# Performance work log

Measured on AMD Instinct MI355X. Metric: run time of the kernel, lower is better.

## Reference

```python
import jax, jax.numpy as jnp
import numpy as np

REF_POSE = np.array([[213.33335876464844, 124.50563049316406], [190.504638671875, 115.11840057373047], [169.9791717529297, 101.77180480957031], [146.72341918945312, 96.25749206542969], [128.86770629882812, 87.2344970703125], [150.34292602539062, 101.61070251464844], [119.29926300048828, 98.73982238769531], [100.03463745117188, 99.74459838867188], [82.62400817871094, 101.2509536743164], [148.91049194335938, 112.71517181396484], [114.37303161621094, 113.20121002197266], [91.90096282958984, 116.49812316894531], [74.75020599365234, 119.37875366210938], [149.59658813476562, 124.09295654296875], [119.72419738769531, 126.36898040771484], [99.59107208251953, 129.40196228027344], [82.82524108886719, 131.584228515625], [154.55911254882812, 135.07681274414062], [133.8833770751953, 140.85983276367188], [120.45906066894531, 145.40306091308594], [106.21541595458984, 150.072265625]], dtype=np.float32)

SCALES = (0.25, 0.5, 1.0)
ORIENTATIONS = (0, 90, 180, 270)
INPUT_SIZE = (256, 256)          # (H, W)
ANCHOR_STRIDE = (1, 1)           # (y_stride, x_stride)
POS_TH = 0.5
KPT_SIGMA = 0.05                 # per-keypoint OKS falloff


def _generate_anchor_poses():
    # scale + rotate ref pose about its centroid -> [A, 21, 2]
    c = REF_POSE.mean(axis=0, keepdims=True)
    out = []
    for s in SCALES:
        for o in ORIENTATIONS:
            th = np.deg2rad(o)
            R = np.array([[np.cos(th), -np.sin(th)], [np.sin(th), np.cos(th)]], dtype=np.float32)
            out.append(c + s * (REF_POSE - c) @ R.T)
    return np.stack(out).astype(np.float32)


def _all_anchors(feat_h, feat_w):
    base = _generate_anchor_poses()                      # [A,21,2]
    w_ratio = INPUT_SIZE[1] / feat_w
    h_ratio = INPUT_SIZE[0] / feat_h
    sx = np.arange(0, feat_w, ANCHOR_STRIDE[1]) * w_ratio
    sy = np.arange(0, feat_h, ANCHOR_STRIDE[0]) * h_ratio
    gx, gy = np.meshgrid(sx, sy)
    shifts = np.stack([gx.ravel(), gy.ravel()], axis=1).astype(np.float32)  # [K,2]
    all_a = base[None, :, :, :] + shifts[:, None, None, :]                  # [K,A,21,2]
    return jnp.asarray(all_a.reshape(-1, 21, 2))                            # [K*A,21,2]


def _pose_oks(anchors, gt):
    # anchors [N,21,2], gt [B,2,21,3] -> OKS sim [B,N,2]
    d2 = jnp.sum((anchors[None, :, None, :, :] - gt[:, None, :, :, :2]) ** 2, axis=-1)  # [B,N,2,21]
    vis = (gt[..., 2] > 0).astype(anchors.dtype)[:, None, :, :]                          # [B,1,2,21]
    xy = gt[..., :2]
    area = jnp.prod(xy.max(axis=2) - xy.min(axis=2), axis=-1)                            # [B,2]
    s2 = jnp.maximum(area, 1.0)[:, None, :, None]                                        # [B,1,2,1]
    k2 = (2.0 * KPT_SIGMA) ** 2
    oks = jnp.exp(-d2 / (2.0 * s2 * k2))
    return jnp.sum(oks * vis, axis=-1) / jnp.maximum(jnp.sum(vis, axis=-1), 1.0)          # [B,N,2]


def setup_inputs() -> dict:
    key = jax.random.key(0)
    k1, k2 = jax.random.split(key)
    B = 16
    xy = jax.random.uniform(k1, (B, 42, 2), dtype=jnp.float32) * 216.0 + 20.0
    vis = jnp.ones((B, 42, 1), dtype=jnp.float32)
    pose_gt = jnp.concatenate([xy, vis], axis=-1)          # [B,42,3]
    hand_type = jnp.ones((B, 2), dtype=jnp.int32)          # both hands present
    return {"pose_gt": pose_gt, "hand_type": hand_type, "feat_h": 64, "feat_w": 64}


def reference(pose_gt, hand_type, feat_h, feat_w):
    all_anchors = _all_anchors(feat_h, feat_w)             # [N,21,2], N=K*A
    inside = jnp.sum((all_anchors[..., 0] >= 0) & (all_anchors[..., 1] >= 0)
                     & (all_anchors[..., 0] < INPUT_SIZE[0])
                     & (all_anchors[..., 1] < INPUT_SIZE[1]), axis=1) == 21  # [N]

    B = pose_gt.shape[0]
    gt = pose_gt.reshape(B, 2, 21, 3)                      # hand 0 = right, hand 1 = left
    sim = _pose_oks(all_anchors, gt)                       # [B,N,2]
    am = jnp.argmax(sim, axis=-1)                          # [B,N]
    mx = jnp.max(sim, axis=-1)                             # [B,N]

    right = (am == 0) & (mx > POS_TH) & (hand_type[:, 0:1] == 1) & inside[None, :]
    left = (am == 1) & (mx > POS_TH) & (hand_type[:, 1:2] == 1) & inside[None, :]
    neg = (~right) & (~left) & inside[None, :]

    # labels channel layout matches source: [:,:,0]=left, [:,:,1]=negative, [:,:,2]=right
    labels = jnp.stack([left, neg, right], axis=-1).astype(pose_gt.dtype)   # [B,N,3]
    labels = jnp.where(inside[None, :, None], labels, jnp.asarray(-1.0, pose_gt.dtype))

    pose_targets = (jnp.where(right[..., None, None], gt[:, 0][:, None], 0.0)
                    + jnp.where(left[..., None, None], gt[:, 1][:, None], 0.0))  # [B,N,21,3]

    offsets = pose_targets[..., :2] - all_anchors[None, :, :, :]             # [B,N,21,2]
    offsets = jnp.where(inside[None, :, None, None], offsets, 0.0)
    return all_anchors, inside, labels, offsets
```

## Files before the change

kernel.cpp:

```cpp
#include <hip/hip_runtime.h>
#include <math.h>

#define NA 49152
#define NB 16
#define ABLOCKS 192
#define EPS 1e-3f
#define OF4B 516096
#define OF4  8257536
#define AF4  516096
#define IF4  12288

__device__ __forceinline__ void st4(float* p, float a, float b, float c, float d) {
  *reinterpret_cast<float4*>(p) = make_float4(a, b, c, d);
}

__constant__ float RP[21][2] = {
  {213.33335876464844f, 124.50563049316406f},
  {190.504638671875f,   115.11840057373047f},
  {169.9791717529297f,  101.77180480957031f},
  {146.72341918945312f, 96.25749206542969f},
  {128.86770629882812f, 87.2344970703125f},
  {150.34292602539062f, 101.61070251464844f},
  {119.29926300048828f, 98.73982238769531f},
  {100.03463745117188f, 99.74459838867188f},
  {82.62400817871094f,  101.2509536743164f},
  {148.91049194335938f, 112.71517181396484f},
  {114.37303161621094f, 113.20121002197266f},
  {91.90096282958984f,  116.49812316894531f},
  {74.75020599365234f,  119.37875366210938f},
  {149.59658813476562f, 124.09295654296875f},
  {119.72419738769531f, 126.36898040771484f},
  {99.59107208251953f,  129.40196228027344f},
  {82.82524108886719f,  131.584228515625f},
  {154.55911254882812f, 135.07681274414062f},
  {133.8833770751953f,  140.85983276367188f},
  {120.45906066894531f, 145.40306091308594f},
  {106.21541595458984f, 150.072265625f}
};

__device__ __forceinline__ void ref_center(float& cx, float& cy) {
  #pragma clang fp contract(off)
  float rx[8], ry[8];
  #pragma unroll
  for (int j = 0; j < 8; ++j) {
    rx[j] = RP[j][0] + RP[j + 8][0];
    ry[j] = RP[j][1] + RP[j + 8][1];
  }
  float sx = ((rx[0] + rx[1]) + (rx[2] + rx[3])) + ((rx[4] + rx[5]) + (rx[6] + rx[7]));
  float sy = ((ry[0] + ry[1]) + (ry[2] + ry[3])) + ((ry[4] + ry[5]) + (ry[6] + ry[7]));
  #pragma unroll
  for (int j = 16; j < 21; ++j) { sx += RP[j][0]; sy += RP[j][1]; }
  cx = sx / 21.0f;
  cy = sy / 21.0f;
}

__device__ __forceinline__ float2 base_pt(int p, int j, float cx, float cy) {
  #pragma clang fp contract(off)
  const int si = p >> 2, oi = p & 3;
  const float s = (si == 0) ? 0.25f : (si == 1 ? 0.5f : 1.0f);
  const float dx = s * (RP[j][0] - cx);
  const float dy = s * (RP[j][1] - cy);
  const float rx = (oi == 0) ? dx : (oi == 1 ? -dy : (oi == 2 ? -dx : dy));
  const float ry = (oi == 0) ? dy : (oi == 1 ? dx : (oi == 2 ? -dy : -dx));
  return make_float2(cx + rx, cy + ry);
}

__global__ __launch_bounds__(256, 5) void k_decide(const float* __restrict__ gt,
                                                   const int* __restrict__ ht,
                                                   float* __restrict__ ol,
                                                   char* __restrict__ codes) {
  __shared__ float2 sb2[252];
  __shared__ float4 sg4[21];
  __shared__ float2 sv2[21];
  __shared__ float sden[2], srden[2], snv[2];
  __shared__ int sht[2];
  __shared__ int scc[256];

  const int tid = threadIdx.x;
  const int b = blockIdx.x / ABLOCKS;
  const int ab = blockIdx.x % ABLOCKS;
  const int a0 = ab * 256;

  if (tid < 252) {
    float cx, cy; ref_center(cx, cy);
    sb2[tid] = base_pt(tid / 21, tid % 21, cx, cy);
  }
  if (tid < 21) {
    const float* g0 = gt + b * 126 + tid * 3;
    const float* g1 = g0 + 63;
    sg4[tid] = make_float4(g0[0], g0[1], g1[0], g1[1]);
    sv2[tid] = make_float2((g0[2] > 0.0f) ? 1.0f : 0.0f,
                           (g1[2] > 0.0f) ? 1.0f : 0.0f);
  }
  if (tid == 252 || tid == 253) {
    const int h = tid - 252;
    const float* g = gt + b * 126 + h * 63;
    float mnx = g[0], mxx = g[0], mny = g[1], mxy = g[1];
    float nv = (g[2] > 0.0f) ? 1.0f : 0.0f;
    for (int j = 1; j < 21; ++j) {
      float x = g[j * 3], y = g[j * 3 + 1];
      mnx = fminf(mnx, x); mxx = fmaxf(mxx, x);
      mny = fminf(mny, y); mxy = fmaxf(mxy, y);
      nv += (g[j * 3 + 2] > 0.0f) ? 1.0f : 0.0f;
    }
    const float area = (mxx - mnx) * (mxy - mny);
    const float s2 = fmaxf(area, 1.0f);
    const float den = (2.0f * s2) * 0.01f;
    sden[h] = den;
    srden[h] = -1.0f / den;
    snv[h] = fmaxf(nv, 1.0f);
  }
  if (tid == 254 || tid == 255) sht[tid - 254] = ht[b * 2 + (tid - 254)];
  __syncthreads();

  const int a = a0 + tid;
  const int p = a % 12;
  const int kc = a / 12;
  const float shx = 4.0f * (float)(kc & 63);
  const float shy = 4.0f * (float)(kc >> 6);
  const int pb = p * 21;

  const float rd0 = srden[0], rd1 = srden[1];
  bool inside = true;
  float s0f = 0.0f, s1f = 0.0f;
  #pragma unroll
  for (int j = 0; j < 21; ++j) {
    #pragma clang fp contract(off)
    const float2 bpv = sb2[pb + j];
    const float anx = bpv.x + shx;
    const float any = bpv.y + shy;
    inside = inside && (anx >= 0.0f) && (any >= 0.0f) &&
                       (anx < 256.0f) && (any < 256.0f);
    const float4 g = sg4[j];
    const float2 v = sv2[j];
    const float dx0 = anx - g.x, dy0 = any - g.y;
    const float dx1 = anx - g.z, dy1 = any - g.w;
    s0f += __expf((dx0 * dx0 + dy0 * dy0) * rd0) * v.x;
    s1f += __expf((dx1 * dx1 + dy1 * dy1) * rd1) * v.y;
  }
  float sim0 = s0f / snv[0];
  float sim1 = s1f / snv[1];
  const float mxf = fmaxf(sim0, sim1);
  const bool need_exact = (fabsf(mxf - 0.5f) < EPS) ||
                          ((mxf > 0.5f - EPS) && (fabsf(sim0 - sim1) < EPS));

  if (__builtin_expect(need_exact, 0)) {
    #pragma clang fp contract(off)
    float q0[8], q1[8];
    #pragma unroll
    for (int j = 0; j < 16; ++j) {
      const float2 bpv = sb2[pb + j];
      const float ax = bpv.x + shx, ay = bpv.y + shy;
      const float4 g = sg4[j];
      const float2 v = sv2[j];
      float dx0 = ax - g.x, dy0 = ay - g.y;
      float d20 = dx0 * dx0 + dy0 * dy0;
      float t0 = (float)::exp((double)(-d20 / sden[0])) * v.x;
      float dx1 = ax - g.z, dy1 = ay - g.w;
      float d21 = dx1 * dx1 + dy1 * dy1;
      float t1 = (float)::exp((double)(-d21 / sden[1])) * v.y;
      if (j < 8) { q0[j] = t0; q1[j] = t1; }
      else       { q0[j - 8] += t0; q1[j - 8] += t1; }
    }
    float s0 = ((q0[0] + q0[1]) + (q0[2] + q0[3])) + ((q0[4] + q0[5]) + (q0[6] + q0[7]));
    float s1 = ((q1[0] + q1[1]) + (q1[2] + q1[3])) + ((q1[4] + q1[5]) + (q1[6] + q1[7]));
    #pragma unroll
    for (int j = 16; j < 21; ++j) {
      const float2 bpv = sb2[pb + j];
      const float ax = bpv.x + shx, ay = bpv.y + shy;
      const float4 g = sg4[j];
      const float2 v = sv2[j];
      float dx0 = ax - g.x, dy0 = ay - g.y;
      float d20 = dx0 * dx0 + dy0 * dy0;
      s0 += (float)::exp((double)(-d20 / sden[0])) * v.x;
      float dx1 = ax - g.z, dy1 = ay - g.w;
      float d21 = dx1 * dx1 + dy1 * dy1;
      s1 += (float)::exp((double)(-d21 / sden[1])) * v.y;
    }
    sim0 = s0 / snv[0];
    sim1 = s1 / snv[1];
  }

  const int am = (sim1 > sim0) ? 1 : 0;
  const float mx = fmaxf(sim0, sim1);
  const bool pos = mx > 0.5f;
  const bool right = (am == 0) && pos && (sht[0] == 1) && inside;
  const bool left  = (am == 1) && pos && (sht[1] == 1) && inside;

  int c;
  if (!inside)      c = -1;
  else if (right)   c = 1;
  else if (left)    c = 2;
  else              c = 0;
  scc[tid] = c;
  codes[b * NA + a] = (char)c;
  __syncthreads();

  if (tid < 192) {
    float* lb = ol + ((size_t)b * NA + a0) * 3;
    float r[4];
    #pragma unroll
    for (int k = 0; k < 4; ++k) {
      const int q = tid * 4 + k;
      const int al = q / 3;
      const int rr = q - al * 3;
      const int cc = scc[al];
      float v;
      if (cc < 0)       v = -1.0f;
      else if (rr == 0) v = (cc == 2) ? 1.0f : 0.0f;
      else if (rr == 1) v = (cc == 0) ? 1.0f : 0.0f;
      else              v = (cc == 1) ? 1.0f : 0.0f;
      r[k] = v;
    }
    st4(lb + tid * 4, r[0], r[1], r[2], r[3]);
  }
}

__device__ __forceinline__ float2 off_elem(int e, const char* __restrict__ codes,
                                           int cb, const float2* sb2,
                                           const float4* sg) {
  #pragma clang fp contract(off)
  const int al = e / 21;
  const int j  = e - al * 21;
  const int kc = al / 12;
  const int p  = al - kc * 12;
  const float shx = 4.0f * (float)(kc & 63);
  const float shy = 4.0f * (float)(kc >> 6);
  const float2 bpv = sb2[p * 21 + j];
  const float anx = bpv.x + shx, any = bpv.y + shy;
  const int cc = (int)codes[cb + al];
  const float4 g = sg[j];
  const bool has = (cc == 1) || (cc == 2);
  float tx = (cc == 2) ? g.z : g.x;
  float ty = (cc == 2) ? g.w : g.y;
  tx = has ? tx : 0.0f; ty = has ? ty : 0.0f;
  return make_float2((cc >= 0) ? (tx - anx) : 0.0f,
                     (cc >= 0) ? (ty - any) : 0.0f);
}

__device__ __forceinline__ float2 anc_elem(int e, const float2* sb2) {
  const int al = e / 21;
  const int j  = e - al * 21;
  const int kc = al / 12;
  const int p  = al - kc * 12;
  const float shx = 4.0f * (float)(kc & 63);
  const float shy = 4.0f * (float)(kc >> 6);
  const float2 bpv = sb2[p * 21 + j];
  return make_float2(bpv.x + shx, bpv.y + shy);
}

__global__ __launch_bounds__(256, 6) void k_stream(const float* __restrict__ gt,
                                                   const char* __restrict__ codes,
                                                   float* __restrict__ oa,
                                                   float* __restrict__ oins,
                                                   float* __restrict__ oo) {
  __shared__ float2 sb2[252];
  __shared__ float4 sgall[NB * 21];

  const int tid = threadIdx.x;
  if (tid < 252) {
    float cx, cy; ref_center(cx, cy);
    sb2[tid] = base_pt(tid / 21, tid % 21, cx, cy);
  }
  for (int t = tid; t < NB * 21; t += 256) {
    const int bb = t / 21, j = t - bb * 21;
    const float* g0 = gt + bb * 126 + j * 3;
    const float* g1 = g0 + 63;
    sgall[t] = make_float4(g0[0], g0[1], g1[0], g1[1]);
  }
  __syncthreads();

  const int G = gridDim.x * 256;
  const int g0i = blockIdx.x * 256 + tid;

  for (int q = g0i; q < OF4; q += G) {
    const int b = q / OF4B;
    const int r = q - b * OF4B;
    const int e0 = 2 * r;
    const float2 r0 = off_elem(e0,     codes, b * NA, sb2, sgall + b * 21);
    const float2 r1 = off_elem(e0 + 1, codes, b * NA, sb2, sgall + b * 21);
    st4(oo + (size_t)q * 4, r0.x, r0.y, r1.x, r1.y);
  }

  for (int q = g0i; q < AF4; q += G) {
    const int e0 = 2 * q;
    const float2 r0 = anc_elem(e0, sb2);
    const float2 r1 = anc_elem(e0 + 1, sb2);
    st4(oa + (size_t)q * 4, r0.x, r0.y, r1.x, r1.y);
  }

  for (int q = g0i; q < IF4; q += G) {
    const char4 c4 = *reinterpret_cast<const char4*>(codes + q * 4);
    st4(oins + (size_t)q * 4,
        (c4.x >= 0) ? 1.0f : 0.0f,
        (c4.y >= 0) ? 1.0f : 0.0f,
        (c4.z >= 0) ? 1.0f : 0.0f,
        (c4.w >= 0) ? 1.0f : 0.0f);
  }
}

extern "C" void kernel_launch(void* const* d_in, const int* in_sizes, int n_in,
                              void* d_out, int out_size, void* d_ws, size_t ws_size,
                              hipStream_t stream) {
  (void)in_sizes; (void)n_in; (void)ws_size; (void)out_size;
  const float* gt = (const float*)d_in[0];
  const int* ht = (const int*)d_in[1];
  float* out = (float*)d_out;
  float* out_anchors = out;
  float* out_inside  = out + (size_t)NA * 42;
  float* out_labels  = out + (size_t)NA * 43;
  float* out_offsets = out_labels + (size_t)NB * NA * 3;
  char* codes = (char*)d_ws;

  hipLaunchKernelGGL(k_decide, dim3(NB * ABLOCKS), dim3(256), 0, stream,
                     gt, ht, out_labels, codes);
  hipLaunchKernelGGL(k_stream, dim3(2048), dim3(256), 0, stream,
                     gt, codes, out_anchors, out_inside, out_offsets);
}
```

Measured before the change: 171.0 us.

## Fill offsets with a shared negative pattern across batches, then patch positive anchors

```diff
diff --git a/kernel.cpp b/kernel.cpp
--- a/kernel.cpp
+++ b/kernel.cpp
@@ -6,8 +6,6 @@
 #define ABLOCKS 192
 #define EPS 1e-3f
 #define OF4B 516096
-#define OF4  8257536
-#define AF4  516096
 #define IF4  12288
 
 __device__ __forceinline__ void st4(float* p, float a, float b, float c, float d) {
@@ -216,86 +214,87 @@
   }
 }
 
-__device__ __forceinline__ float2 off_elem(int e, const char* __restrict__ codes,
-                                           int cb, const float2* sb2,
-                                           const float4* sg) {
-  #pragma clang fp contract(off)
-  const int al = e / 21;
-  const int j  = e - al * 21;
-  const int kc = al / 12;
-  const int p  = al - kc * 12;
-  const float shx = 4.0f * (float)(kc & 63);
-  const float shy = 4.0f * (float)(kc >> 6);
-  const float2 bpv = sb2[p * 21 + j];
-  const float anx = bpv.x + shx, any = bpv.y + shy;
-  const int cc = (int)codes[cb + al];
-  const float4 g = sg[j];
-  const bool has = (cc == 1) || (cc == 2);
-  float tx = (cc == 2) ? g.z : g.x;
-  float ty = (cc == 2) ? g.w : g.y;
-  tx = has ? tx : 0.0f; ty = has ? ty : 0.0f;
-  return make_float2((cc >= 0) ? (tx - anx) : 0.0f,
-                     (cc >= 0) ? (ty - any) : 0.0f);
-}
-
-__device__ __forceinline__ float2 anc_elem(int e, const float2* sb2) {
-  const int al = e / 21;
-  const int j  = e - al * 21;
-  const int kc = al / 12;
-  const int p  = al - kc * 12;
-  const float shx = 4.0f * (float)(kc & 63);
-  const float shy = 4.0f * (float)(kc >> 6);
-  const float2 bpv = sb2[p * 21 + j];
-  return make_float2(bpv.x + shx, bpv.y + shy);
-}
-
-__global__ __launch_bounds__(256, 6) void k_stream(const float* __restrict__ gt,
-                                                   const char* __restrict__ codes,
-                                                   float* __restrict__ oa,
-                                                   float* __restrict__ oins,
-                                                   float* __restrict__ oo) {
+__global__ __launch_bounds__(256) void k_bulk(const char* __restrict__ codes,
+                                              float* __restrict__ oa,
+                                              float* __restrict__ oins,
+                                              float* __restrict__ oo) {
   __shared__ float2 sb2[252];
-  __shared__ float4 sgall[NB * 21];
-
   const int tid = threadIdx.x;
   if (tid < 252) {
     float cx, cy; ref_center(cx, cy);
     sb2[tid] = base_pt(tid / 21, tid % 21, cx, cy);
   }
-  for (int t = tid; t < NB * 21; t += 256) {
-    const int bb = t / 21, j = t - bb * 21;
-    const float* g0 = gt + bb * 126 + j * 3;
-    const float* g1 = g0 + 63;
-    sgall[t] = make_float4(g0[0], g0[1], g1[0], g1[1]);
-  }
   __syncthreads();
 
-  const int G = gridDim.x * 256;
-  const int g0i = blockIdx.x * 256 + tid;
-
-  for (int q = g0i; q < OF4; q += G) {
-    const int b = q / OF4B;
-    const int r = q - b * OF4B;
-    const int e0 = 2 * r;
-    const float2 r0 = off_elem(e0,     codes, b * NA, sb2, sgall + b * 21);
-    const float2 r1 = off_elem(e0 + 1, codes, b * NA, sb2, sgall + b * 21);
-    st4(oo + (size_t)q * 4, r0.x, r0.y, r1.x, r1.y);
-  }
-
-  for (int q = g0i; q < AF4; q += G) {
-    const int e0 = 2 * q;
-    const float2 r0 = anc_elem(e0, sb2);
-    const float2 r1 = anc_elem(e0 + 1, sb2);
-    st4(oa + (size_t)q * 4, r0.x, r0.y, r1.x, r1.y);
-  }
-
-  for (int q = g0i; q < IF4; q += G) {
+  const int q = blockIdx.x * 256 + tid;
+  const int e0 = 2 * q;
+  const int al = e0 / 21;
+  const int j  = e0 - al * 21;
+  const bool w1 = (j + 1) >= 21;
+  const int al1 = al + (w1 ? 1 : 0);
+  const int j1 = w1 ? 0 : (j + 1);
+
+  const int kc0 = al / 12, p0 = al - kc0 * 12;
+  const int kc1 = al1 / 12, p1 = al1 - kc1 * 12;
+  float ax0, ay0, ax1, ay1;
+  {
+    #pragma clang fp contract(off)
+    const float2 b0 = sb2[p0 * 21 + j];
+    const float2 b1 = sb2[p1 * 21 + j1];
+    ax0 = b0.x + 4.0f * (float)(kc0 & 63);
+    ay0 = b0.y + 4.0f * (float)(kc0 >> 6);
+    ax1 = b1.x + 4.0f * (float)(kc1 & 63);
+    ay1 = b1.y + 4.0f * (float)(kc1 >> 6);
+  }
+  const bool in0 = codes[al] >= 0;
+  const bool in1 = codes[al1] >= 0;
+
+  const float4 A = make_float4(ax0, ay0, ax1, ay1);
+  const float4 O = make_float4(in0 ? -ax0 : 0.0f, in0 ? -ay0 : 0.0f,
+                               in1 ? -ax1 : 0.0f, in1 ? -ay1 : 0.0f);
+
+  reinterpret_cast<float4*>(oa)[q] = A;
+  float4* oo4 = reinterpret_cast<float4*>(oo);
+  #pragma unroll
+  for (int b = 0; b < NB; ++b)
+    oo4[q + b * OF4B] = O;
+
+  if (q < IF4) {
     const char4 c4 = *reinterpret_cast<const char4*>(codes + q * 4);
     st4(oins + (size_t)q * 4,
         (c4.x >= 0) ? 1.0f : 0.0f,
         (c4.y >= 0) ? 1.0f : 0.0f,
         (c4.z >= 0) ? 1.0f : 0.0f,
         (c4.w >= 0) ? 1.0f : 0.0f);
+  }
+}
+
+__global__ __launch_bounds__(256) void k_patch(const float* __restrict__ gt,
+                                               const char* __restrict__ codes,
+                                               float* __restrict__ oo) {
+  const int t = blockIdx.x * 256 + threadIdx.x;
+  const char4 c4 = *reinterpret_cast<const char4*>(codes + t * 4);
+  const char cs[4] = {c4.x, c4.y, c4.z, c4.w};
+  #pragma unroll
+  for (int k = 0; k < 4; ++k) {
+    const int cc = (int)cs[k];
+    if (__builtin_expect(cc == 1 || cc == 2, 0)) {
+      const int i = t * 4 + k;
+      const int b = i / NA;
+      const int a = i - b * NA;
+      const float* g = gt + b * 126 + ((cc == 2) ? 63 : 0);
+      const int p = a % 12, kc = a / 12;
+      const float shx = 4.0f * (float)(kc & 63);
+      const float shy = 4.0f * (float)(kc >> 6);
+      float cx, cy; ref_center(cx, cy);
+      float* row = oo + (size_t)i * 42;
+      for (int j = 0; j < 21; ++j) {
+        #pragma clang fp contract(off)
+        const float2 bp = base_pt(p, j, cx, cy);
+        row[2 * j]     = g[j * 3]     - (bp.x + shx);
+        row[2 * j + 1] = g[j * 3 + 1] - (bp.y + shy);
+      }
+    }
   }
 }
 
@@ -314,6 +313,8 @@
 
   hipLaunchKernelGGL(k_decide, dim3(NB * ABLOCKS), dim3(256), 0, stream,
                      gt, ht, out_labels, codes);
-  hipLaunchKernelGGL(k_stream, dim3(2048), dim3(256), 0, stream,
-                     gt, codes, out_anchors, out_inside, out_offsets);
-}
+  hipLaunchKernelGGL(k_bulk, dim3(2016), dim3(256), 0, stream,
+                     codes, out_anchors, out_inside, out_offsets);
+  hipLaunchKernelGGL(k_patch, dim3(768), dim3(256), 0, stream,
+                     gt, codes, out_offsets);
+}
```

After: 176.1 us. +3.0%, slower.
